# Kernel optimization log

Measured on AMD Instinct MI355X. Metric: run time of the kernel, lower is better.

The kernel has to match this reference:

```python
import jax, jax.numpy as jnp
import numpy as np

DIM = 1024
HIDDEN = 2048
NUM_EXPERTS = 8
TOP_K = 2


def setup_inputs() -> dict:
    key = jax.random.key(0)
    ks = jax.random.split(key, 6)
    scale = 0.02
    x = jax.random.normal(ks[0], (2, 4096, DIM), dtype=jnp.float32)
    # router: Linear(dim, num_experts, bias=False) -> weight [E, d]
    router_w = jax.random.normal(ks[1], (NUM_EXPERTS, DIM), dtype=jnp.float32) * scale
    # per-expert MLP: Linear(d, h) -> w1 [E, h, d], b1 [E, h]; Linear(h, d) -> w2 [E, d, h], b2 [E, d]
    w1 = jax.random.normal(ks[2], (NUM_EXPERTS, HIDDEN, DIM), dtype=jnp.float32) * scale
    b1 = jnp.zeros((NUM_EXPERTS, HIDDEN), dtype=jnp.float32)
    w2 = jax.random.normal(ks[3], (NUM_EXPERTS, DIM, HIDDEN), dtype=jnp.float32) * scale
    b2 = jnp.zeros((NUM_EXPERTS, DIM), dtype=jnp.float32)
    return {"x": x, "router_w": router_w, "w1": w1, "b1": b1, "w2": w2, "b2": b2}


def reference(x, router_w, w1, b1, w2, b2):
    b, s, d = x.shape
    xf = x.reshape(-1, d)                              # [T, d]
    logits = xf @ router_w.T                           # [T, E]
    all_probs = jax.nn.softmax(logits, axis=-1)
    topk_logits, topk_inds = jax.lax.top_k(logits, TOP_K)   # [T, K]
    topk_probs = jax.nn.softmax(topk_logits, axis=-1)
    E = router_w.shape[0]
    onehot = jax.nn.one_hot(topk_inds, E, dtype=xf.dtype)   # [T, K, E]
    # combine weights per (token, expert); zero where expert not selected
    gate = jnp.einsum('tke,tk->te', onehot, topk_probs)     # [T, E]
    # load-balancing auxiliary loss
    f_i = onehot.mean(axis=(0, 1))                          # [E]
    P_i = all_probs.mean(axis=0)                            # [E]
    aux_loss = E * jnp.sum(f_i * P_i)
    # dense per-expert MLP, weighted combine (dropout=0 / eval mode)
    out = jnp.zeros_like(xf)
    for e in range(E):  # fixed small loop over experts
        h = jax.nn.gelu(xf @ w1[e].T + b1[e], approximate=False)  # exact GELU (torch default)
        y = h @ w2[e].T + b2[e]
        out = out + gate[:, e:e + 1] * y
    return out.reshape(b, s, d), aux_loss
```

## Files before the change

### kernel.cpp

```cpp
#include <hip/hip_runtime.h>


#define TOKS 8192
#define DIMD 1024
#define HID  2048
#define NE   8

#define OFF_COUNTS   0
#define OFF_OFFSETS  64
#define OFF_CURSORS  128
#define OFF_TILEOFF  192
#define OFF_TOPKI    256
#define OFF_TOPKG    (OFF_TOPKI + TOKS*2*4)
#define OFF_BLKPS    (OFF_TOPKG + TOKS*2*4)
#define OFF_ATOK     (OFF_BLKPS + 2048*NE*4)
#define OFF_AGATE    (OFF_ATOK + TOKS*2*4)
#define OFF_PINV     (OFF_AGATE + TOKS*2*4)
#define OFF_XG       (1u << 20)
#define XG_ROWS      (TOKS*2 + 256)
#define OFF_W1B      (OFF_XG  + (size_t)XG_ROWS * DIMD * 2)
#define OFF_W2B      (OFF_W1B + (size_t)NE * HID * DIMD * 2)
#define OFF_H        (OFF_W2B + (size_t)NE * DIMD * HID * 2)
#define OFF_Y        (OFF_H   + (size_t)XG_ROWS * HID * 2)

typedef __bf16 bf16x8 __attribute__((ext_vector_type(8)));
typedef float  floatx4 __attribute__((ext_vector_type(4)));

__device__ __forceinline__ float bf2f(unsigned short u) {
    return __uint_as_float(((unsigned)u) << 16);
}
__device__ __forceinline__ unsigned short f2bf(float f) {
    unsigned u = __float_as_uint(f);
    unsigned r = (u + 0x7FFFu + ((u >> 16) & 1u)) >> 16;
    return (unsigned short)r;
}

#define GLOBAL_AS(p) ((const __attribute__((address_space(1))) unsigned int*)(p))
#define LDS_AS(p)    ((__attribute__((address_space(3))) unsigned int*)(p))

__device__ __forceinline__ int xcd_remap(int bid, int nwg) {
    int xcd = bid & 7, pos = bid >> 3;
    int q = nwg >> 3, r = nwg & 7;
    int start = (xcd < r) ? xcd * (q + 1) : r * (q + 1) + (xcd - r) * q;
    return start + pos;
}

__global__ void convert_w_kernel(const float4* __restrict__ w1,
                                 ushort4* __restrict__ w1b, int n1,
                                 const float4* __restrict__ w2,
                                 ushort4* __restrict__ w2b, int n2) {
    int i = blockIdx.x * blockDim.x + threadIdx.x;
    int stride = gridDim.x * blockDim.x;
    int ntot = n1 + n2;
    for (; i < ntot; i += stride) {
        float4 v; ushort4 o;
        if (i < n1) v = w1[i]; else v = w2[i - n1];
        o.x = f2bf(v.x); o.y = f2bf(v.y); o.z = f2bf(v.z); o.w = f2bf(v.w);
        if (i < n1) w1b[i] = o; else w2b[i - n1] = o;
    }
}

__global__ __launch_bounds__(256) void router_kernel(
    const float* __restrict__ x, const float* __restrict__ rw,
    int* __restrict__ topki, float* __restrict__ topkg,
    float* __restrict__ blkps)
{
    int wave = threadIdx.x >> 6;
    int lane = threadIdx.x & 63;
    int t = blockIdx.x * 4 + wave;
    const float* xt = x + (size_t)t * DIMD;

    float acc[NE];
#pragma unroll
    for (int e = 0; e < NE; e++) acc[e] = 0.f;
    for (int i = 0; i < DIMD / 64; i++) {
        float xv = xt[lane + 64 * i];
#pragma unroll
        for (int e = 0; e < NE; e++) acc[e] += xv * rw[e * DIMD + lane + 64 * i];
    }
#pragma unroll
    for (int off = 32; off > 0; off >>= 1) {
#pragma unroll
        for (int e = 0; e < NE; e++) acc[e] += __shfl_down(acc[e], off);
    }

    __shared__ float ps[4][NE];
    if (lane == 0) {
        float m = acc[0];
#pragma unroll
        for (int e = 1; e < NE; e++) m = fmaxf(m, acc[e]);
        float ex[NE], s = 0.f;
#pragma unroll
        for (int e = 0; e < NE; e++) { ex[e] = expf(acc[e] - m); s += ex[e]; }
        float inv = 1.f / s;
#pragma unroll
        for (int e = 0; e < NE; e++) ps[wave][e] = ex[e] * inv;

        int i0 = 0; float l0 = acc[0];
#pragma unroll
        for (int e = 1; e < NE; e++) if (acc[e] > l0) { l0 = acc[e]; i0 = e; }
        int i1 = -1; float l1 = -3.4e38f;
#pragma unroll
        for (int e = 0; e < NE; e++) if (e != i0 && acc[e] > l1) { l1 = acc[e]; i1 = e; }
        float e1 = expf(l1 - l0);
        float g0 = 1.f / (1.f + e1);
        float g1 = e1 * g0;
        topki[t * 2 + 0] = i0; topki[t * 2 + 1] = i1;
        topkg[t * 2 + 0] = g0; topkg[t * 2 + 1] = g1;
    }
    __syncthreads();
    if (threadIdx.x < NE) {
        float s = ps[0][threadIdx.x] + ps[1][threadIdx.x] + ps[2][threadIdx.x] + ps[3][threadIdx.x];
        blkps[blockIdx.x * NE + threadIdx.x] = s;
    }
}

__global__ __launch_bounds__(256) void finalize_kernel(
    const int* __restrict__ topki, const float* __restrict__ blkps,
    int* __restrict__ counts, int* __restrict__ offsets, int* __restrict__ cursors,
    int* __restrict__ tileoff, float* __restrict__ aux_out)
{
    __shared__ float psum[NE];
    __shared__ int cnt[NE];
    int tid = threadIdx.x;
    if (tid < NE) { psum[tid] = 0.f; cnt[tid] = 0; }
    __syncthreads();

    float lp[NE]; int lc[NE];
#pragma unroll
    for (int e = 0; e < NE; e++) { lp[e] = 0.f; lc[e] = 0; }
    const float4* bp4 = (const float4*)blkps;
    for (int i = tid; i < 2048 * NE / 4; i += 256) {
        float4 v = bp4[i];
        int eb = (4 * i) & 7;
        lp[eb + 0] += v.x; lp[eb + 1] += v.y; lp[eb + 2] += v.z; lp[eb + 3] += v.w;
    }
    const int4* ti4 = (const int4*)topki;
    for (int i = tid; i < TOKS * 2 / 4; i += 256) {
        int4 v = ti4[i];
        lc[v.x]++; lc[v.y]++; lc[v.z]++; lc[v.w]++;
    }
#pragma unroll
    for (int e = 0; e < NE; e++) { atomicAdd(&psum[e], lp[e]); atomicAdd(&cnt[e], lc[e]); }
    __syncthreads();

    if (tid == 0) {
        int off = 0, to = 0;
        for (int e = 0; e < NE; e++) {
            counts[e] = cnt[e];
            offsets[e] = off; cursors[e] = off;
            tileoff[e] = to;
            off += cnt[e];
            to += (cnt[e] + 255) >> 8;
        }
        offsets[NE] = off; tileoff[NE] = to;
        float aux = 0.f;
        for (int e = 0; e < NE; e++)
            aux += ((float)cnt[e] / (float)(TOKS * 2)) * (psum[e] / (float)TOKS);
        aux_out[0] = (float)NE * aux;
    }
}

__global__ __launch_bounds__(64) void fill_kernel(
    const int* __restrict__ topki, const float* __restrict__ topkg,
    int* __restrict__ cursors, int* __restrict__ atok, float* __restrict__ agate,
    int* __restrict__ posinv)
{
    int lane = threadIdx.x;
    int t = blockIdx.x * 64 + lane;
    unsigned long long below = (lane == 63) ? 0x7FFFFFFFFFFFFFFFull
                                            : ((1ull << lane) - 1ull);
#pragma unroll
    for (int k = 0; k < 2; k++) {
        int e = topki[t * 2 + k];
        float g = topkg[t * 2 + k];
        for (int ee = 0; ee < NE; ee++) {
            bool pred = (e == ee);
            unsigned long long mask = __ballot(pred ? 1 : 0);
            if (mask) {
                int leader = __ffsll((unsigned long long)mask) - 1;
                int base = 0;
                if (lane == leader) base = atomicAdd(&cursors[ee], (int)__popcll(mask));
                base = __shfl(base, leader);
                if (pred) {
                    int pos = base + (int)__popcll(mask & below);
                    atok[pos] = t;
                    agate[pos] = g;
                    posinv[t * 2 + k] = pos;
                }
            }
        }
    }
}

__global__ __launch_bounds__(256) void gather_x_kernel(
    const float* __restrict__ x, const int* __restrict__ posinv,
    ushort* __restrict__ Xg)
{
    int t = blockIdx.x;
    int tid = threadIdx.x;
    float4 v = ((const float4*)(x + (size_t)t * DIMD))[tid];
    ushort4 o;
    o.x = f2bf(v.x); o.y = f2bf(v.y); o.z = f2bf(v.z); o.w = f2bf(v.w);
    int p0 = posinv[t * 2 + 0], p1 = posinv[t * 2 + 1];
    ((ushort4*)(Xg + (size_t)p0 * DIMD))[tid] = o;
    ((ushort4*)(Xg + (size_t)p1 * DIMD))[tid] = o;
}

template<int LD, int NT>
__device__ __forceinline__ void gemm_tlp(
    const ushort* __restrict__ gApanel, const ushort* __restrict__ gBpanel,
    ushort (&lds)[2][24][512], floatx4 (&acc)[4][4],
    int lane, int wave, int wr, int wc, int l15, int quad)
{
    auto stage = [&](int bsel, int u) {
#pragma unroll
        for (int t = 0; t < 2; t++) {
            int s = wave * 2 + t;
            const ushort* a0 = gApanel + (size_t)(s * 16 + l15) * LD + u * 32 + quad * 8;
            __builtin_amdgcn_global_load_lds(GLOBAL_AS(a0),
                LDS_AS(&lds[bsel][s][0]), 16, 0, 0);
        }
        const ushort* b0 = gBpanel + (size_t)(wave * 16 + l15) * LD + u * 32 + quad * 8;
        __builtin_amdgcn_global_load_lds(GLOBAL_AS(b0),
            LDS_AS(&lds[bsel][16 + wave][0]), 16, 0, 0);
    };

#pragma unroll
    for (int i = 0; i < 4; i++)
#pragma unroll
        for (int j = 0; j < 4; j++) acc[i][j] = (floatx4){0.f, 0.f, 0.f, 0.f};

    stage(0, 0);
    __syncthreads();

    for (int u = 0; u < NT; u++) {
        if (u + 1 < NT) stage((u + 1) & 1, u + 1);
        const bf16x8* C = (const bf16x8*)&lds[u & 1][0][0];
        bf16x8 a[4], b[4];
#pragma unroll
        for (int mi = 0; mi < 4; mi++) a[mi] = C[(wr * 4 + mi) * 64 + lane];
#pragma unroll
        for (int nj = 0; nj < 4; nj++) b[nj] = C[(16 + wc * 4 + nj) * 64 + lane];
#pragma unroll
        for (int mi = 0; mi < 4; mi++)
#pragma unroll
            for (int nj = 0; nj < 4; nj++)
                acc[mi][nj] = __builtin_amdgcn_mfma_f32_16x16x32_bf16(
                    a[mi], b[nj], acc[mi][nj], 0, 0, 0);
        __syncthreads();
    }
}

__global__ __launch_bounds__(512, 4) void phase1_kernel(
    const ushort* __restrict__ Xg, const ushort* __restrict__ w1b,
    const float* __restrict__ b1,
    const int* __restrict__ counts, const int* __restrict__ offsets,
    const int* __restrict__ tileoff, unsigned short* __restrict__ Hbuf)
{
    const int NCOLT = HID / 128;
    int total = tileoff[NE] * NCOLT;
    int idx = xcd_remap((int)blockIdx.x, (int)gridDim.x);
    if (idx >= total) return;
    int ct = idx & (NCOLT - 1);
    int rowt = idx / NCOLT;
    int e = 0;
    while (rowt >= tileoff[e + 1]) e++;
    int row0 = (rowt - tileoff[e]) * 256;
    int cnt = counts[e];
    int base = offsets[e];
    int colbase = ct * 128;

    __shared__ ushort lds[2][24][512];

    int tid = threadIdx.x;
    int lane = tid & 63;
    int wave = tid >> 6;
    int wr = wave >> 1, wc = wave & 1;
    int l15 = lane & 15, quad = lane >> 4;

    const ushort* gApanel = Xg + (size_t)(base + row0) * DIMD;
    const ushort* gBpanel = w1b + (size_t)e * HID * DIMD + (size_t)colbase * DIMD;

    floatx4 acc[4][4];
    gemm_tlp<DIMD, DIMD / 32>(gApanel, gBpanel, lds, acc, lane, wave, wr, wc, l15, quad);

    float b1v[4];
#pragma unroll
    for (int j = 0; j < 4; j++)
        b1v[j] = b1[e * HID + colbase + 64 * wc + 16 * j + l15];
#pragma unroll
    for (int i = 0; i < 4; i++) {
#pragma unroll
        for (int rr = 0; rr < 4; rr++) {
            int pr = row0 + 64 * wr + 16 * i + quad * 4 + rr;
            if (pr < cnt) {
                size_t hrow = (size_t)(base + pr) * HID;
#pragma unroll
                for (int j = 0; j < 4; j++) {
                    int col = colbase + 64 * wc + 16 * j + l15;
                    float v = acc[i][j][rr] + b1v[j];
                    v = 0.5f * v * (1.f + erff(v * 0.70710678118654752f));
                    Hbuf[hrow + col] = f2bf(v);
                }
            }
        }
    }
}

__global__ __launch_bounds__(512, 4) void phase2_kernel(
    const ushort* __restrict__ Hbuf, const ushort* __restrict__ w2b,
    const int* __restrict__ counts, const int* __restrict__ offsets,
    const int* __restrict__ tileoff, ushort* __restrict__ Y)
{
    const int NCOLT = DIMD / 128;
    int total = tileoff[NE] * NCOLT;
    int idx = xcd_remap((int)blockIdx.x, (int)gridDim.x);
    if (idx >= total) return;
    int ct = idx & (NCOLT - 1);
    int rowt = idx / NCOLT;
    int e = 0;
    while (rowt >= tileoff[e + 1]) e++;
    int row0 = (rowt - tileoff[e]) * 256;
    int cnt = counts[e];
    int base = offsets[e];
    int colbase = ct * 128;

    __shared__ ushort lds[2][24][512];

    int tid = threadIdx.x;
    int lane = tid & 63;
    int wave = tid >> 6;
    int wr = wave >> 1, wc = wave & 1;
    int l15 = lane & 15, quad = lane >> 4;

    const ushort* gApanel = Hbuf + (size_t)(base + row0) * HID;
    const ushort* gBpanel = w2b + (size_t)e * DIMD * HID + (size_t)colbase * HID;

    floatx4 acc[4][4];
    gemm_tlp<HID, HID / 32>(gApanel, gBpanel, lds, acc, lane, wave, wr, wc, l15, quad);

#pragma unroll
    for (int i = 0; i < 4; i++) {
#pragma unroll
        for (int rr = 0; rr < 4; rr++) {
            int pr = row0 + 64 * wr + 16 * i + quad * 4 + rr;
            if (pr < cnt) {
                size_t yrow = (size_t)(base + pr) * DIMD;
#pragma unroll
                for (int j = 0; j < 4; j++) {
                    int col = colbase + 64 * wc + 16 * j + l15;
                    Y[yrow + col] = f2bf(acc[i][j][rr]);
                }
            }
        }
    }
}

__global__ __launch_bounds__(256) void combine_kernel(
    const ushort* __restrict__ Y, const float* __restrict__ b2,
    const int* __restrict__ topki, const float* __restrict__ topkg,
    const int* __restrict__ posinv, float* __restrict__ out)
{
    int wave = threadIdx.x >> 6;
    int lane = threadIdx.x & 63;
    int t = blockIdx.x * 4 + wave;
    int e0 = topki[t * 2 + 0], e1 = topki[t * 2 + 1];
    float g0 = topkg[t * 2 + 0], g1 = topkg[t * 2 + 1];
    int p0 = posinv[t * 2 + 0], p1 = posinv[t * 2 + 1];

    const ushort4* y0 = (const ushort4*)(Y + (size_t)p0 * DIMD);
    const ushort4* y1 = (const ushort4*)(Y + (size_t)p1 * DIMD);
    const float4* b20 = (const float4*)(b2 + (size_t)e0 * DIMD);
    const float4* b21 = (const float4*)(b2 + (size_t)e1 * DIMD);
    float4* o4 = (float4*)(out + (size_t)t * DIMD);

#pragma unroll
    for (int c = 0; c < DIMD / 4 / 64; c++) {
        int i = lane + 64 * c;
        ushort4 a = y0[i], b = y1[i];
        float4 ba = b20[i], bb = b21[i];
        float4 r;
        r.x = g0 * (bf2f(a.x) + ba.x) + g1 * (bf2f(b.x) + bb.x);
        r.y = g0 * (bf2f(a.y) + ba.y) + g1 * (bf2f(b.y) + bb.y);
        r.z = g0 * (bf2f(a.z) + ba.z) + g1 * (bf2f(b.z) + bb.z);
        r.w = g0 * (bf2f(a.w) + ba.w) + g1 * (bf2f(b.w) + bb.w);
        o4[i] = r;
    }
}

extern "C" void kernel_launch(void* const* d_in, const int* in_sizes, int n_in,
                              void* d_out, int out_size, void* d_ws, size_t ws_size,
                              hipStream_t stream) {
    const float* x  = (const float*)d_in[0];
    const float* rw = (const float*)d_in[1];
    const float* w1 = (const float*)d_in[2];
    const float* b1 = (const float*)d_in[3];
    const float* w2 = (const float*)d_in[4];
    const float* b2 = (const float*)d_in[5];
    float* out = (float*)d_out;

    char* ws = (char*)d_ws;
    int*   counts  = (int*)(ws + OFF_COUNTS);
    int*   offsets = (int*)(ws + OFF_OFFSETS);
    int*   cursors = (int*)(ws + OFF_CURSORS);
    int*   tileoff = (int*)(ws + OFF_TILEOFF);
    int*   topki   = (int*)(ws + OFF_TOPKI);
    float* topkg   = (float*)(ws + OFF_TOPKG);
    float* blkps   = (float*)(ws + OFF_BLKPS);
    int*   atok    = (int*)(ws + OFF_ATOK);
    float* agate   = (float*)(ws + OFF_AGATE);
    int*   posinv  = (int*)(ws + OFF_PINV);
    ushort* Xg     = (ushort*)(ws + OFF_XG);
    ushort* w1b    = (ushort*)(ws + OFF_W1B);
    ushort* w2b    = (ushort*)(ws + OFF_W2B);
    ushort* Hbuf   = (ushort*)(ws + OFF_H);
    ushort* Y      = (ushort*)(ws + OFF_Y);

    convert_w_kernel<<<8192, 256, 0, stream>>>(
        (const float4*)w1, (ushort4*)w1b, NE * HID * DIMD / 4,
        (const float4*)w2, (ushort4*)w2b, NE * DIMD * HID / 4);

    router_kernel<<<TOKS / 4, 256, 0, stream>>>(x, rw, topki, topkg, blkps);
    finalize_kernel<<<1, 256, 0, stream>>>(topki, blkps, counts, offsets, cursors,
                                           tileoff, out + (size_t)TOKS * DIMD);
    fill_kernel<<<TOKS / 64, 64, 0, stream>>>(topki, topkg, cursors, atok, agate,
                                              posinv);
    gather_x_kernel<<<TOKS, 256, 0, stream>>>(x, posinv, Xg);

    phase1_kernel<<<71 * (HID / 128), 512, 0, stream>>>(
        Xg, w1b, b1, counts, offsets, tileoff, Hbuf);
    phase2_kernel<<<71 * (DIMD / 128), 512, 0, stream>>>(
        Hbuf, w2b, counts, offsets, tileoff, Y);
    combine_kernel<<<TOKS / 4, 256, 0, stream>>>(Y, b2, topki, topkg, posinv, out);
}
```

Measured before the change: 592.8 us.

## Retile expert down-projection to 128x128 blocks and group phase1 tiles for L2 reuse

The second expert GEMM now uses 128-row tiles computed by 256-thread blocks through a new 4-wave staging helper. `finalize_kernel` emits a second prefix of per-expert tile offsets at 128-row granularity to support this. The change roughly doubles the number of blocks so the GPU's many CUs stay busier in that GEMM. The first GEMM's block index is remapped into 4x8 supertiles so nearby blocks share activation rows and weight columns in L2. The trade-off is smaller tiles in phase2, which lowers arithmetic intensity per block and reloads weights more often.

```diff
diff --git a/kernel.cpp b/kernel.cpp
--- a/kernel.cpp
+++ b/kernel.cpp
@@ -10,7 +10,8 @@
 #define OFF_OFFSETS  64
 #define OFF_CURSORS  128
 #define OFF_TILEOFF  192
-#define OFF_TOPKI    256
+#define OFF_T128     240
+#define OFF_TOPKI    320
 #define OFF_TOPKG    (OFF_TOPKI + TOKS*2*4)
 #define OFF_BLKPS    (OFF_TOPKG + TOKS*2*4)
 #define OFF_ATOK     (OFF_BLKPS + 2048*NE*4)
@@ -118,7 +119,8 @@
 __global__ __launch_bounds__(256) void finalize_kernel(
     const int* __restrict__ topki, const float* __restrict__ blkps,
     int* __restrict__ counts, int* __restrict__ offsets, int* __restrict__ cursors,
-    int* __restrict__ tileoff, float* __restrict__ aux_out)
+    int* __restrict__ tileoff, int* __restrict__ tileoff128,
+    float* __restrict__ aux_out)
 {
     __shared__ float psum[NE];
     __shared__ int cnt[NE];
@@ -145,15 +147,17 @@
     __syncthreads();
 
     if (tid == 0) {
-        int off = 0, to = 0;
+        int off = 0, to = 0, to1 = 0;
         for (int e = 0; e < NE; e++) {
             counts[e] = cnt[e];
             offsets[e] = off; cursors[e] = off;
             tileoff[e] = to;
+            tileoff128[e] = to1;
             off += cnt[e];
-            to += (cnt[e] + 255) >> 8;
-        }
-        offsets[NE] = off; tileoff[NE] = to;
+            to  += (cnt[e] + 255) >> 8;
+            to1 += (cnt[e] + 127) >> 7;
+        }
+        offsets[NE] = off; tileoff[NE] = to; tileoff128[NE] = to1;
         float aux = 0.f;
         for (int e = 0; e < NE; e++)
             aux += ((float)cnt[e] / (float)(TOKS * 2)) * (psum[e] / (float)TOKS);
@@ -252,18 +256,65 @@
     }
 }
 
+template<int LD, int NT>
+__device__ __forceinline__ void gemm_tlp4(
+    const ushort* __restrict__ gApanel, const ushort* __restrict__ gBpanel,
+    ushort (&lds)[2][16][512], floatx4 (&acc)[4][4],
+    int lane, int wave, int wr, int wc, int l15, int quad)
+{
+    auto stage = [&](int bsel, int u) {
+#pragma unroll
+        for (int t = 0; t < 4; t++) {
+            int c = wave * 4 + t;
+            const ushort* p = (c < 8)
+                ? gApanel + (size_t)(c * 16 + l15) * LD + u * 32 + quad * 8
+                : gBpanel + (size_t)((c - 8) * 16 + l15) * LD + u * 32 + quad * 8;
+            __builtin_amdgcn_global_load_lds(GLOBAL_AS(p),
+                LDS_AS(&lds[bsel][c][0]), 16, 0, 0);
+        }
+    };
+
+#pragma unroll
+    for (int i = 0; i < 4; i++)
+#pragma unroll
+        for (int j = 0; j < 4; j++) acc[i][j] = (floatx4){0.f, 0.f, 0.f, 0.f};
+
+    stage(0, 0);
+    __syncthreads();
+
+    for (int u = 0; u < NT; u++) {
+        if (u + 1 < NT) stage((u + 1) & 1, u + 1);
+        const bf16x8* C = (const bf16x8*)&lds[u & 1][0][0];
+        bf16x8 a[4], b[4];
+#pragma unroll
+        for (int mi = 0; mi < 4; mi++) a[mi] = C[(wr * 4 + mi) * 64 + lane];
+#pragma unroll
+        for (int nj = 0; nj < 4; nj++) b[nj] = C[(8 + wc * 4 + nj) * 64 + lane];
+#pragma unroll
+        for (int mi = 0; mi < 4; mi++)
+#pragma unroll
+            for (int nj = 0; nj < 4; nj++)
+                acc[mi][nj] = __builtin_amdgcn_mfma_f32_16x16x32_bf16(
+                    a[mi], b[nj], acc[mi][nj], 0, 0, 0);
+        __syncthreads();
+    }
+}
+
 __global__ __launch_bounds__(512, 4) void phase1_kernel(
     const ushort* __restrict__ Xg, const ushort* __restrict__ w1b,
     const float* __restrict__ b1,
     const int* __restrict__ counts, const int* __restrict__ offsets,
     const int* __restrict__ tileoff, unsigned short* __restrict__ Hbuf)
 {
-    const int NCOLT = HID / 128;
-    int total = tileoff[NE] * NCOLT;
-    int idx = xcd_remap((int)blockIdx.x, (int)gridDim.x);
-    if (idx >= total) return;
-    int ct = idx & (NCOLT - 1);
-    int rowt = idx / NCOLT;
+    int T1 = tileoff[NE];
+    int T1p = (T1 + 3) & ~3;
+    int g = xcd_remap((int)blockIdx.x, (int)gridDim.x);
+    if (g >= T1p * 16) return;
+    int s = g >> 5, u = g & 31;
+    int srow = s >> 1, scol = s & 1;
+    int rowt = srow * 4 + (u >> 3);
+    int ct   = scol * 8 + (u & 7);
+    if (rowt >= T1) return;
     int e = 0;
     while (rowt >= tileoff[e + 1]) e++;
     int row0 = (rowt - tileoff[e]) * 256;
@@ -308,25 +359,28 @@
     }
 }
 
-__global__ __launch_bounds__(512, 4) void phase2_kernel(
+__global__ __launch_bounds__(256, 4) void phase2_kernel(
     const ushort* __restrict__ Hbuf, const ushort* __restrict__ w2b,
     const int* __restrict__ counts, const int* __restrict__ offsets,
-    const int* __restrict__ tileoff, ushort* __restrict__ Y)
-{
-    const int NCOLT = DIMD / 128;
-    int total = tileoff[NE] * NCOLT;
-    int idx = xcd_remap((int)blockIdx.x, (int)gridDim.x);
-    if (idx >= total) return;
-    int ct = idx & (NCOLT - 1);
-    int rowt = idx / NCOLT;
+    const int* __restrict__ t128, ushort* __restrict__ Y)
+{
+    int T2 = t128[NE];
+    int T2p = (T2 + 3) & ~3;
+    int g = xcd_remap((int)blockIdx.x, (int)gridDim.x);
+    if (g >= T2p * 8) return;
+    int s = g >> 4, u = g & 15;
+    int srow = s >> 1, scol = s & 1;
+    int rowt = srow * 4 + (u >> 2);
+    int ct   = scol * 4 + (u & 3);
+    if (rowt >= T2) return;
     int e = 0;
-    while (rowt >= tileoff[e + 1]) e++;
-    int row0 = (rowt - tileoff[e]) * 256;
+    while (rowt >= t128[e + 1]) e++;
+    int row0 = (rowt - t128[e]) * 128;
     int cnt = counts[e];
     int base = offsets[e];
     int colbase = ct * 128;
 
-    __shared__ ushort lds[2][24][512];
+    __shared__ ushort lds[2][16][512];
 
     int tid = threadIdx.x;
     int lane = tid & 63;
@@ -338,7 +392,7 @@
     const ushort* gBpanel = w2b + (size_t)e * DIMD * HID + (size_t)colbase * HID;
 
     floatx4 acc[4][4];
-    gemm_tlp<HID, HID / 32>(gApanel, gBpanel, lds, acc, lane, wave, wr, wc, l15, quad);
+    gemm_tlp4<HID, HID / 32>(gApanel, gBpanel, lds, acc, lane, wave, wr, wc, l15, quad);
 
 #pragma unroll
     for (int i = 0; i < 4; i++) {
@@ -405,6 +459,7 @@
     int*   offsets = (int*)(ws + OFF_OFFSETS);
     int*   cursors = (int*)(ws + OFF_CURSORS);
     int*   tileoff = (int*)(ws + OFF_TILEOFF);
+    int*   t128    = (int*)(ws + OFF_T128);
     int*   topki   = (int*)(ws + OFF_TOPKI);
     float* topkg   = (float*)(ws + OFF_TOPKG);
     float* blkps   = (float*)(ws + OFF_BLKPS);
@@ -423,14 +478,15 @@
 
     router_kernel<<<TOKS / 4, 256, 0, stream>>>(x, rw, topki, topkg, blkps);
     finalize_kernel<<<1, 256, 0, stream>>>(topki, blkps, counts, offsets, cursors,
-                                           tileoff, out + (size_t)TOKS * DIMD);
+                                           tileoff, t128,
+                                           out + (size_t)TOKS * DIMD);
     fill_kernel<<<TOKS / 64, 64, 0, stream>>>(topki, topkg, cursors, atok, agate,
                                               posinv);
     gather_x_kernel<<<TOKS, 256, 0, stream>>>(x, posinv, Xg);
 
-    phase1_kernel<<<71 * (HID / 128), 512, 0, stream>>>(
+    phase1_kernel<<<1152, 512, 0, stream>>>(
         Xg, w1b, b1, counts, offsets, tileoff, Hbuf);
-    phase2_kernel<<<71 * (DIMD / 128), 512, 0, stream>>>(
-        Hbuf, w2b, counts, offsets, tileoff, Y);
+    phase2_kernel<<<1088, 256, 0, stream>>>(
+        Hbuf, w2b, counts, offsets, t128, Y);
     combine_kernel<<<TOKS / 4, 256, 0, stream>>>(Y, b2, topki, topkg, posinv, out);
 }
```

Result: slower. 650.8 us (+9.8%).
